# Kernel tuning notes

Hardware: AMD Instinct MI355X
Metric: run time of the kernel (lower is better)

The kernel has to match this reference:

```python
import jax, jax.numpy as jnp
import numpy as np

B, N, DX, DZ, L = 512, 32, 78, 64, 1000

def _gcn_norm(A):
    # PyG gcn_norm: add remaining self loops (fill 1), symmetric D^-1/2 (A+I) D^-1/2
    n = A.shape[-1]
    A_hat = jnp.maximum(A, jnp.eye(n, dtype=A.dtype))
    dinv = jax.lax.rsqrt(A_hat.sum(-1))
    return A_hat * dinv[..., :, None] * dinv[..., None, :]

def _bn(h, g, b, eps=1e-5):
    # BatchNorm1d, training-mode batch statistics (torch default module state)
    m = jnp.mean(h, 0)
    v = jnp.var(h, 0)
    return (h - m) * jax.lax.rsqrt(v + eps) * g + b

def _conv(h, W, b):  # h [B,C,L], W [O,I,K], valid padding + ReLU (Conv1dReLU)
    y = jax.lax.conv_general_dilated(h, W, (1,), 'VALID', dimension_numbers=('NCH', 'OIH', 'NCH'))
    return jax.nn.relu(y + b[None, :, None])

def _attn(v):  # Attention.project is only Tanh in the source
    return jax.nn.softmax(jnp.tanh(v), axis=1) * v

def _forward(x, adj, target, z, dec_W0, dec_b0, dec_g0, dec_be0, dec_W1, dec_b1, dec_g1, dec_be1,
             gW1, gb1, gW2, gb2, gW3, gb3, fcg1_W, fcg1_b, fcg2_W, fcg2_b, emb,
             c10_W, c10_b, c20_W, c20_b, c21_W, c21_b, c30_W, c30_b, c31_W, c31_b, c32_W, c32_b,
             prot_W, prot_b, fc1_W, fc1_b, fc2_W, fc2_b, out_W, out_b):
    Bn = B * N
    # frozen conditional VAE decoder -> augmented features (detached)
    zc = jnp.concatenate([z.reshape(Bn, DZ), x.reshape(Bn, DX)], axis=-1)
    h = jax.nn.relu(_bn(zc @ dec_W0 + dec_b0, dec_g0, dec_be0))
    aug = jnp.tanh(_bn(h @ dec_W1 + dec_b1, dec_g1, dec_be1))
    aug = jax.lax.stop_gradient(aug).reshape(B, N, DX)
    X = jnp.concatenate([aug, x], axis=-1)  # [B,N,156]
    # 1-hop / 2-hop / 3-hop adjacency patterns (spspmm -> binary power patterns)
    A1 = _gcn_norm(adj)
    A2p = (adj @ adj > 0).astype(adj.dtype)
    A3p = (A2p @ adj > 0).astype(adj.dtype)
    A2 = _gcn_norm(A2p)
    A3 = _gcn_norm(A3p)
    gcn = lambda A, hh, W, b: jax.nn.relu(A @ (hh @ W) + b)
    h1 = gcn(A1, X, gW1, gb1)
    h2 = gcn(A1, h1, gW2, gb2)
    h3 = gcn(A1, h2, gW3, gb3)
    h5 = gcn(A2, gcn(A2, X, gW1, gb1), gW2, gb2)
    h6 = gcn(A3, X, gW1, gb1)
    hg = jnp.max(jnp.concatenate([h3, h5, h6], axis=-1), axis=1)  # gmp -> [B,1092]
    xg = jax.nn.relu(hg @ fcg1_W + fcg1_b) @ fcg2_W + fcg2_b  # dropout = identity (eval)
    xg = _attn(xg)
    # protein branch
    e = jnp.transpose(emb[target], (0, 2, 1))  # [B,128,1000]
    f1 = jnp.max(_conv(e, c10_W, c10_b), axis=-1)
    f2 = jnp.max(_conv(_conv(e, c20_W, c20_b), c21_W, c21_b), axis=-1)
    f3 = jnp.max(_conv(_conv(_conv(e, c30_W, c30_b), c31_W, c31_b), c32_W, c32_b), axis=-1)
    xt = _attn(jnp.concatenate([f1, f2, f3], axis=-1) @ prot_W + prot_b)
    xc = jnp.concatenate([xg, xt], axis=-1)
    xc = jax.nn.relu(xc @ fc1_W + fc1_b)
    xc = jax.nn.relu(xc @ fc2_W + fc2_b)
    return xc @ out_W + out_b

def setup_inputs():
    key = jax.random.key(0)
    ks = iter(jax.random.split(key, 64))
    def w(shape, s=0.05):
        return jax.random.normal(next(ks), shape, dtype=jnp.float32) * s
    x = jax.random.normal(next(ks), (B, N, DX), dtype=jnp.float32)
    r = jax.random.uniform(next(ks), (B, N, N))
    up = jnp.triu((r < 0.08).astype(jnp.float32), 1)
    adj = up + jnp.swapaxes(up, 1, 2)  # symmetric, no self loops, avg degree ~5
    target = jax.random.randint(next(ks), (B, L), 0, 26, dtype=jnp.int32)
    z = jax.random.normal(next(ks), (B, N, DZ), dtype=jnp.float32)
    emb = w((26, 128), 1.0).at[0].set(0.0)  # padding_idx=0
    return dict(x=x, adj=adj, target=target, z=z,
        dec_W0=w((DZ + DX, 256)), dec_b0=jnp.zeros(256), dec_g0=jnp.ones(256), dec_be0=jnp.zeros(256),
        dec_W1=w((256, DX)), dec_b1=jnp.zeros(DX), dec_g1=jnp.ones(DX), dec_be1=jnp.zeros(DX),
        gW1=w((156, 156)), gb1=jnp.zeros(156), gW2=w((156, 312)), gb2=jnp.zeros(312),
        gW3=w((312, 624)), gb3=jnp.zeros(624),
        fcg1_W=w((1092, 1024)), fcg1_b=jnp.zeros(1024), fcg2_W=w((1024, 128)), fcg2_b=jnp.zeros(128),
        emb=emb,
        c10_W=w((96, 128, 3)), c10_b=jnp.zeros(96),
        c20_W=w((96, 128, 3)), c20_b=jnp.zeros(96), c21_W=w((96, 96, 3)), c21_b=jnp.zeros(96),
        c30_W=w((96, 128, 3)), c30_b=jnp.zeros(96), c31_W=w((96, 96, 3)), c31_b=jnp.zeros(96),
        c32_W=w((96, 96, 3)), c32_b=jnp.zeros(96),
        prot_W=w((288, 128)), prot_b=jnp.zeros(128),
        fc1_W=w((256, 1024)), fc1_b=jnp.zeros(1024), fc2_W=w((1024, 512)), fc2_b=jnp.zeros(512),
        out_W=w((512, 1)), out_b=jnp.zeros(1))

def reference(x, adj, target, z, dec_W0, dec_b0, dec_g0, dec_be0, dec_W1, dec_b1, dec_g1, dec_be1,
              gW1, gb1, gW2, gb2, gW3, gb3, fcg1_W, fcg1_b, fcg2_W, fcg2_b, emb,
              c10_W, c10_b, c20_W, c20_b, c21_W, c21_b, c30_W, c30_b, c31_W, c31_b, c32_W, c32_b,
              prot_W, prot_b, fc1_W, fc1_b, fc2_W, fc2_b, out_W, out_b):
    return _forward(x, adj, target, z, dec_W0, dec_b0, dec_g0, dec_be0, dec_W1, dec_b1, dec_g1, dec_be1,
                    gW1, gb1, gW2, gb2, gW3, gb3, fcg1_W, fcg1_b, fcg2_W, fcg2_b, emb,
                    c10_W, c10_b, c20_W, c20_b, c21_W, c21_b, c30_W, c30_b, c31_W, c31_b, c32_W, c32_b,
                    prot_W, prot_b, fc1_W, fc1_b, fc2_W, fc2_b, out_W, out_b)
```

## Files before the change

kernel.cpp:

```cpp
#include <hip/hip_runtime.h>

static constexpr size_t O_H0    = 0;
static constexpr size_t O_H1P   = 4194304;
static constexpr size_t O_X     = 5473216;
static constexpr size_t O_A1    = 8029120;
static constexpr size_t O_A2    = 8553408;
static constexpr size_t O_A3    = 9077696;
static constexpr size_t O_H4    = 9601984;
static constexpr size_t O_H6    = 12157888;
static constexpr size_t O_H1W2  = 14713792;
static constexpr size_t O_H2    = 19825600;
static constexpr size_t O_H2W3  = 24937408;
static constexpr size_t O_H3    = 35161024;
static constexpr size_t O_HG    = 45384640;
static constexpr size_t O_FCG1O = 45943744;
static constexpr size_t O_M     = 46468032;
static constexpr size_t O_F     = 46535424;
static constexpr size_t O_V     = 46682880;
static constexpr size_t O_XC    = 46748416;
static constexpr size_t O_FC1O  = 46879488;
static constexpr size_t O_FC2O  = 47403776;
static constexpr size_t O_PART  = 47665920;
static constexpr size_t O_MV    = 47698688;
static constexpr size_t O_BT21  = 47699712;
static constexpr size_t O_BT31  = 47727360;
static constexpr size_t O_W32T  = 47755008;
static constexpr size_t O_XW1  = O_H0;
static constexpr size_t O_SK   = O_H0;
static constexpr size_t O_H1   = O_X;
static constexpr size_t O_H4W2 = O_H1W2;
static constexpr size_t O_H5   = O_H2W3;
static constexpr size_t O_R10  = O_H1W2;
static constexpr size_t O_R20  = O_H1W2 + 1687296;
static constexpr size_t O_R30  = O_H1W2 + 3374592;
static constexpr size_t O_N21  = O_H2W3;
static constexpr size_t O_N31  = O_H2W3 + 5061888;

template<int AMODE, int ACT>
__global__ __launch_bounds__(256) void gemm_k(
    const float* __restrict__ A, const float* __restrict__ Bm,
    const float* __restrict__ bias, float* __restrict__ C,
    int M, int N, int K, const float* __restrict__ A2)
{
  __shared__ __align__(16) float sA[16 * 68];
  __shared__ __align__(16) float sB[16 * 68];
  const int tid = threadIdx.x;
  const int m0 = blockIdx.y * 64, n0 = blockIdx.x * 64;
  const int tx = tid & 15, ty = tid >> 4;
  float acc[4][4] = {};
  for (int k0 = 0; k0 < K; k0 += 16) {
#pragma unroll
    for (int s2 = 0; s2 < 4; s2++) {
      int idx = tid + s2 * 256;
      int am = idx >> 4, ak = idx & 15;
      int gm = m0 + am, gk = k0 + ak;
      float va = 0.f;
      if (gm < M && gk < K) {
        if (AMODE == 0) va = A[(size_t)gm * K + gk];
        else            va = (gk < 64) ? A[gm * 64 + gk] : A2[gm * 78 + gk - 64];
      }
      sA[ak * 68 + am] = va;
      int bk2 = idx >> 6, bn = idx & 63;
      int gk2 = k0 + bk2, gn = n0 + bn;
      float vb = 0.f;
      if (gk2 < K && gn < N) vb = Bm[(size_t)gk2 * N + gn];
      sB[bk2 * 68 + bn] = vb;
    }
    __syncthreads();
#pragma unroll
    for (int kk = 0; kk < 16; kk++) {
      const float4 a4 = *(const float4*)&sA[kk * 68 + ty * 4];
      const float4 b4 = *(const float4*)&sB[kk * 68 + tx * 4];
      const float ra[4] = {a4.x, a4.y, a4.z, a4.w};
      const float rb[4] = {b4.x, b4.y, b4.z, b4.w};
#pragma unroll
      for (int i2 = 0; i2 < 4; i2++)
#pragma unroll
        for (int j2 = 0; j2 < 4; j2++)
          acc[i2][j2] = fmaf(ra[i2], rb[j2], acc[i2][j2]);
    }
    __syncthreads();
  }
#pragma unroll
  for (int i2 = 0; i2 < 4; i2++) {
    int gm = m0 + ty * 4 + i2;
    if (gm >= M) continue;
#pragma unroll
    for (int j2 = 0; j2 < 4; j2++) {
      int gn = n0 + tx * 4 + j2;
      if (gn >= N) continue;
      float v = acc[i2][j2];
      if (bias) v += bias[gn];
      if (ACT == 1) v = fmaxf(v, 0.f);
      C[(size_t)gm * N + gn] = v;
    }
  }
}

__global__ __launch_bounds__(256) void gemm_sk(
    const float* __restrict__ A, const float* __restrict__ Bm,
    float* __restrict__ PT, int M, int N, int K, int KS)
{
  __shared__ __align__(16) float sA[16 * 68];
  __shared__ __align__(16) float sB[16 * 68];
  const int tid = threadIdx.x;
  const int m0 = blockIdx.y * 64, n0 = blockIdx.x * 64;
  const int kb = blockIdx.z * KS;
  const int ke = min(K, kb + KS);
  const int tx = tid & 15, ty = tid >> 4;
  float acc[4][4] = {};
  for (int k0 = kb; k0 < ke; k0 += 16) {
#pragma unroll
    for (int s2 = 0; s2 < 4; s2++) {
      int idx = tid + s2 * 256;
      int am = idx >> 4, ak = idx & 15;
      int gm = m0 + am, gk = k0 + ak;
      float va = 0.f;
      if (gm < M && gk < ke) va = A[(size_t)gm * K + gk];
      sA[ak * 68 + am] = va;
      int bk2 = idx >> 6, bn = idx & 63;
      int gk2 = k0 + bk2, gn = n0 + bn;
      float vb = 0.f;
      if (gk2 < ke && gn < N) vb = Bm[(size_t)gk2 * N + gn];
      sB[bk2 * 68 + bn] = vb;
    }
    __syncthreads();
#pragma unroll
    for (int kk = 0; kk < 16; kk++) {
      const float4 a4 = *(const float4*)&sA[kk * 68 + ty * 4];
      const float4 b4 = *(const float4*)&sB[kk * 68 + tx * 4];
      const float ra[4] = {a4.x, a4.y, a4.z, a4.w};
      const float rb[4] = {b4.x, b4.y, b4.z, b4.w};
#pragma unroll
      for (int i2 = 0; i2 < 4; i2++)
#pragma unroll
        for (int j2 = 0; j2 < 4; j2++)
          acc[i2][j2] = fmaf(ra[i2], rb[j2], acc[i2][j2]);
    }
    __syncthreads();
  }
  float* P = PT + (size_t)blockIdx.z * M * N;
#pragma unroll
  for (int i2 = 0; i2 < 4; i2++) {
    int gm = m0 + ty * 4 + i2;
    if (gm >= M) continue;
#pragma unroll
    for (int j2 = 0; j2 < 4; j2++) {
      int gn = n0 + tx * 4 + j2;
      if (gn >= N) continue;
      P[(size_t)gm * N + gn] = acc[i2][j2];
    }
  }
}

__global__ void skred_kernel(const float* __restrict__ PT, const float* __restrict__ bias,
                             float* __restrict__ C, int MN, int nmask, int S, int act)
{
  int i = blockIdx.x * 256 + threadIdx.x;
  if (i >= MN) return;
  float s = 0.f;
  for (int z = 0; z < S; z++) s += PT[(size_t)z * MN + i];
  if (bias) s += bias[i & nmask];
  if (act) s = fmaxf(s, 0.f);
  C[i] = s;
}

template<int AMODE, int ACT>
__global__ __launch_bounds__(256) void gemm2_k(
    const float* __restrict__ A, const float* __restrict__ Bm,
    const float* __restrict__ bias, float* __restrict__ C,
    int M, int N, int K, const float* __restrict__ A2)
{
  __shared__ __align__(16) float sA[16 * 132];
  __shared__ __align__(16) float sB[16 * 68];
  const int tid = threadIdx.x;
  const int m0 = blockIdx.y * 128, n0 = blockIdx.x * 64;
  const int tx = tid & 15, ty = tid >> 4;
  float acc[8][4] = {};
  for (int k0 = 0; k0 < K; k0 += 16) {
#pragma unroll
    for (int s2 = 0; s2 < 2; s2++) {
      int idx = tid + s2 * 256;
      int am = idx >> 2, kq = idx & 3;
      int gm = m0 + am;
#pragma unroll
      for (int j = 0; j < 4; j++) {
        int gk = k0 + kq * 4 + j;
        float va = 0.f;
        if (gm < M && gk < K) {
          if (AMODE == 0) va = A[(size_t)gm * K + gk];
          else            va = (gk < 64) ? A[gm * 64 + gk] : A2[gm * 78 + gk - 64];
        }
        sA[(kq * 4 + j) * 132 + am] = va;
      }
    }
    {
      int bk = tid >> 4, bn4 = tid & 15;
      int gk2 = k0 + bk;
#pragma unroll
      for (int j = 0; j < 4; j++) {
        int gn = n0 + bn4 * 4 + j;
        float vb = 0.f;
        if (gk2 < K && gn < N) vb = Bm[(size_t)gk2 * N + gn];
        sB[bk * 68 + bn4 * 4 + j] = vb;
      }
    }
    __syncthreads();
#pragma unroll
    for (int kk = 0; kk < 16; kk++) {
      const float4 a0 = *(const float4*)&sA[kk * 132 + ty * 8];
      const float4 a1 = *(const float4*)&sA[kk * 132 + ty * 8 + 4];
      const float4 b4 = *(const float4*)&sB[kk * 68 + tx * 4];
      const float ra[8] = {a0.x, a0.y, a0.z, a0.w, a1.x, a1.y, a1.z, a1.w};
      const float rb[4] = {b4.x, b4.y, b4.z, b4.w};
#pragma unroll
      for (int i2 = 0; i2 < 8; i2++)
#pragma unroll
        for (int j2 = 0; j2 < 4; j2++)
          acc[i2][j2] = fmaf(ra[i2], rb[j2], acc[i2][j2]);
    }
    __syncthreads();
  }
#pragma unroll
  for (int i2 = 0; i2 < 8; i2++) {
    int gm = m0 + ty * 8 + i2;
    if (gm >= M) continue;
#pragma unroll
    for (int j2 = 0; j2 < 4; j2++) {
      int gn = n0 + tx * 4 + j2;
      if (gn >= N) continue;
      float v = acc[i2][j2];
      if (bias) v += bias[gn];
      if (ACT == 1) v = fmaxf(v, 0.f);
      C[(size_t)gm * N + gn] = v;
    }
  }
}

template<int AMODE, int ACT>
__global__ __launch_bounds__(256) void gemm3_k(
    const float* __restrict__ A, const float* __restrict__ Bm,
    const float* __restrict__ bias, float* __restrict__ C,
    int M, int N, int K, const float* __restrict__ A2)
{
  __shared__ __align__(16) float sA[16][132];
  __shared__ __align__(16) float sB[16][132];
  const int tid = threadIdx.x;
  const int m0 = blockIdx.y * 128, n0 = blockIdx.x * 128;
  const int tx = tid & 15, ty = tid >> 4;
  float acc[8][8] = {};
  for (int k0 = 0; k0 < K; k0 += 16) {
    {
      int am = tid >> 1;
      int kq = (tid & 1) * 8;
      int gm = m0 + am;
#pragma unroll
      for (int j = 0; j < 8; j++) {
        int gk = k0 + kq + j;
        float va = 0.f;
        if (gm < M && gk < K) {
          if (AMODE == 0) va = A[(size_t)gm * K + gk];
          else            va = (gk < 64) ? A[gm * 64 + gk] : A2[gm * 78 + gk - 64];
        }
        sA[kq + j][am] = va;
      }
      int bk = tid >> 4;
      int bn = (tid & 15) * 8;
      int gk2 = k0 + bk;
#pragma unroll
      for (int j = 0; j < 8; j++) {
        int gn = n0 + bn + j;
        float vb = 0.f;
        if (gk2 < K && gn < N) vb = Bm[(size_t)gk2 * N + gn];
        sB[bk][bn + j] = vb;
      }
    }
    __syncthreads();
#pragma unroll
    for (int kk = 0; kk < 16; kk++) {
      const float4 a0 = *(const float4*)&sA[kk][ty * 4];
      const float4 a1 = *(const float4*)&sA[kk][64 + ty * 4];
      const float4 b0 = *(const float4*)&sB[kk][tx * 4];
      const float4 b1 = *(const float4*)&sB[kk][64 + tx * 4];
      const float ra[8] = {a0.x, a0.y, a0.z, a0.w, a1.x, a1.y, a1.z, a1.w};
      const float rb[8] = {b0.x, b0.y, b0.z, b0.w, b1.x, b1.y, b1.z, b1.w};
#pragma unroll
      for (int i = 0; i < 8; i++)
#pragma unroll
        for (int j = 0; j < 8; j++)
          acc[i][j] = fmaf(ra[i], rb[j], acc[i][j]);
    }
    __syncthreads();
  }
#pragma unroll
  for (int i = 0; i < 8; i++) {
    int gm = m0 + (i < 4 ? ty * 4 + i : 64 + ty * 4 + (i - 4));
    if (gm >= M) continue;
#pragma unroll
    for (int j = 0; j < 8; j++) {
      int gn = n0 + (j < 4 ? tx * 4 + j : 64 + tx * 4 + (j - 4));
      if (gn >= N) continue;
      float v = acc[i][j];
      if (bias) v += bias[gn];
      if (ACT == 1) v = fmaxf(v, 0.f);
      C[(size_t)gm * N + gn] = v;
    }
  }
}

__global__ __launch_bounds__(256) void bn_partial(const float* __restrict__ H,
    float* __restrict__ PS, float* __restrict__ PQ, int C)
{
  int c = blockIdx.x * 64 + (threadIdx.x & 63);
  int rg = threadIdx.x >> 6;
  __shared__ float sS[256], sQ[256];
  float s = 0.f, q = 0.f;
  if (c < C) {
    int base = blockIdx.y * 256 + rg;
    for (int t = 0; t < 64; t++) {
      float v = H[(size_t)(base + 4 * t) * C + c];
      s += v; q += v * v;
    }
  }
  sS[threadIdx.x] = s; sQ[threadIdx.x] = q;
  __syncthreads();
  if (threadIdx.x < 64 && c < C) {
    float ts = sS[threadIdx.x] + sS[threadIdx.x + 64] + sS[threadIdx.x + 128] + sS[threadIdx.x + 192];
    float tq = sQ[threadIdx.x] + sQ[threadIdx.x + 64] + sQ[threadIdx.x + 128] + sQ[threadIdx.x + 192];
    PS[blockIdx.y * C + c] = ts;
    PQ[blockIdx.y * C + c] = tq;
  }
}

__global__ void bn_final(const float* __restrict__ PS, const float* __restrict__ PQ,
                         float* __restrict__ MV, int C)
{
  int c = threadIdx.x;
  if (c >= C) return;
  float s = 0.f, q = 0.f;
  for (int y = 0; y < 64; y++) { s += PS[y * C + c]; q += PQ[y * C + c]; }
  float mean = s * (1.f / 16384.f);
  float var = q * (1.f / 16384.f) - mean * mean;
  MV[c] = mean; MV[256 + c] = var;
}

__global__ void bn_norm(const float* __restrict__ IN, float* __restrict__ OUT,
                        const float* __restrict__ MV, const float* __restrict__ g,
                        const float* __restrict__ bb, int C, int ostride, int total, int act)
{
  int idx = blockIdx.x * 256 + threadIdx.x;
  if (idx >= total) return;
  int r = idx / C, c = idx - r * C;
  float v = (IN[idx] - MV[c]) * (1.f / sqrtf(MV[256 + c] + 1e-5f)) * g[c] + bb[c];
  v = (act == 1) ? fmaxf(v, 0.f) : tanhf(v);
  OUT[(size_t)r * ostride + c] = v;
}

__global__ void xcopy_kernel(const float* __restrict__ x, float* __restrict__ X)
{
  int idx = blockIdx.x * 256 + threadIdx.x;
  if (idx >= 16384 * 78) return;
  int r = idx / 78, j = idx - r * 78;
  X[(size_t)r * 156 + 78 + j] = x[idx];
}

__global__ __launch_bounds__(1024) void adj_kernel(const float* __restrict__ adj,
    float* __restrict__ A1o, float* __restrict__ A2o, float* __restrict__ A3o)
{
  int b = blockIdx.x, t = threadIdx.x;
  int i = t >> 5, j = t & 31;
  __shared__ float sA[32][33], sP[32][33];
  __shared__ float sd1[32], sd2[32], sd3[32];
  float a = adj[b * 1024 + t];
  sA[i][j] = a;
  float ah = (i == j) ? fmaxf(a, 1.f) : a;
  float rs = ah;
#pragma unroll
  for (int m = 16; m >= 1; m >>= 1) rs += __shfl_xor(rs, m, 32);
  float di = 1.f / sqrtf(rs);
  if (j == 0) sd1[i] = di;
  __syncthreads();
  A1o[b * 1024 + t] = ah * di * sd1[j];
  float c2 = 0.f;
#pragma unroll
  for (int k = 0; k < 32; k++) c2 += sA[i][k] * sA[k][j];
  float p2 = (c2 > 0.f) ? 1.f : 0.f;
  sP[i][j] = p2;
  float ah2 = (i == j) ? 1.f : p2;
  float rs2 = ah2;
#pragma unroll
  for (int m = 16; m >= 1; m >>= 1) rs2 += __shfl_xor(rs2, m, 32);
  float di2 = 1.f / sqrtf(rs2);
  if (j == 0) sd2[i] = di2;
  __syncthreads();
  A2o[b * 1024 + t] = ah2 * di2 * sd2[j];
  float c3 = 0.f;
#pragma unroll
  for (int k = 0; k < 32; k++) c3 += sP[i][k] * sA[k][j];
  float p3 = (c3 > 0.f) ? 1.f : 0.f;
  float ah3 = (i == j) ? 1.f : p3;
  float rs3 = ah3;
#pragma unroll
  for (int m = 16; m >= 1; m >>= 1) rs3 += __shfl_xor(rs3, m, 32);
  float di3 = 1.f / sqrtf(rs3);
  if (j == 0) sd3[i] = di3;
  __syncthreads();
  A3o[b * 1024 + t] = ah3 * di3 * sd3[j];
}

__global__ __launch_bounds__(64) void agg_kernel(const float* __restrict__ A,
    const float* __restrict__ HW, const float* __restrict__ bias,
    float* __restrict__ OUT, int C)
{
  int b = blockIdx.y;
  int c = blockIdx.x * 64 + threadIdx.x;
  __shared__ float sAd[1024];
  for (int e = threadIdx.x; e < 1024; e += 64) sAd[e] = A[b * 1024 + e];
  __syncthreads();
  if (c >= C) return;
  float hw[32];
  const float* hp = HW + (size_t)b * 32 * C + c;
#pragma unroll
  for (int m = 0; m < 32; m++) hw[m] = hp[(size_t)m * C];
  float bv = bias[c];
#pragma unroll 2
  for (int n = 0; n < 32; n++) {
    float s = bv;
#pragma unroll
    for (int m = 0; m < 32; m++) s = fmaf(sAd[n * 32 + m], hw[m], s);
    OUT[(size_t)b * 32 * C + (size_t)n * C + c] = fmaxf(s, 0.f);
  }
}

__global__ void hg_kernel(const float* __restrict__ h3, const float* __restrict__ h5,
                          const float* __restrict__ h6, float* __restrict__ HG)
{
  int b = blockIdx.y;
  int c = blockIdx.x * 256 + threadIdx.x;
  if (c >= 1092) return;
  const float* p; int stride;
  if (c < 624)      { p = h3 + (size_t)b * 32 * 624 + c;          stride = 624; }
  else if (c < 936) { p = h5 + (size_t)b * 32 * 312 + (c - 624);  stride = 312; }
  else              { p = h6 + (size_t)b * 32 * 156 + (c - 936);  stride = 156; }
  float m = p[0];
#pragma unroll 4
  for (int n = 1; n < 32; n++) m = fmaxf(m, p[(size_t)n * stride]);
  HG[b * 1092 + c] = m;
}

__global__ __launch_bounds__(64) void attn_kernel(const float* __restrict__ V,
    float* __restrict__ OUT, int ostride, int ooff)
{
  int r = blockIdx.x, lane = threadIdx.x;
  float v0 = V[r * 128 + lane], v1 = V[r * 128 + 64 + lane];
  float e0 = expf(tanhf(v0)), e1 = expf(tanhf(v1));
  float s = e0 + e1;
#pragma unroll
  for (int m = 32; m >= 1; m >>= 1) s += __shfl_xor(s, m);
  float inv = 1.f / s;
  OUT[r * ostride + ooff + lane] = e0 * inv * v0;
  OUT[r * ostride + ooff + 64 + lane] = e1 * inv * v1;
}

__global__ void mtable_kernel(const float* __restrict__ emb, const float* __restrict__ W10,
    const float* __restrict__ W20, const float* __restrict__ W30, float* __restrict__ M)
{
  int idx = blockIdx.x * 256 + threadIdx.x;
  if (idx >= 3 * 3 * 26 * 96) return;
  int o = idx % 96, tok = (idx / 96) % 26, k = (idx / (96 * 26)) % 3, cv = idx / (96 * 26 * 3);
  const float* W = (cv == 0) ? W10 : ((cv == 1) ? W20 : W30);
  float s = 0.f;
#pragma unroll 4
  for (int i = 0; i < 128; i++) s = fmaf(emb[tok * 128 + i], W[(o * 128 + i) * 3 + k], s);
  M[idx] = s;
}

__global__ void rtable_kernel(const float* __restrict__ M,
    const float* __restrict__ b1, const float* __restrict__ b2, const float* __restrict__ b3,
    float* __restrict__ R1, float* __restrict__ R2, float* __restrict__ R3)
{
  int cv = blockIdx.y;
  int idx = blockIdx.x * 256 + threadIdx.x;
  if (idx >= 17576 * 96) return;
  int o = idx % 96, g = idx / 96;
  int t0 = g / 676, t1 = (g / 26) % 26, t2 = g % 26;
  const float* Mc = M + cv * 3 * 26 * 96;
  float v = ((cv == 0) ? b1 : ((cv == 1) ? b2 : b3))[o];
  v += Mc[(0 * 26 + t0) * 96 + o] + Mc[(1 * 26 + t1) * 96 + o] + Mc[(2 * 26 + t2) * 96 + o];
  float* R = (cv == 0) ? R1 : ((cv == 1) ? R2 : R3);
  R[idx] = fmaxf(v, 0.f);
}

__global__ void wtrans_kernel(const float* __restrict__ W, float* __restrict__ out, int mode)
{
  int e = blockIdx.x * 256 + threadIdx.x;
  if (e >= 96 * 96 * 3) return;
  int o, i, k;
  if (mode == 0) { i = e / 288; int r = e % 288; k = r / 96; o = r % 96; }
  else           { k = e / (96 * 96); i = (e / 96) % 96; o = e % 96; }
  out[e] = W[(o * 96 + i) * 3 + k];
}

__global__ __launch_bounds__(128) void fmax12_scan(const int* __restrict__ target,
    const float* __restrict__ R10, const float* __restrict__ N21, const float* __restrict__ b21,
    float* __restrict__ F)
{
  int b = blockIdx.x;
  const int CH = 125;
  int l0 = blockIdx.y * CH;
  int n1 = min(998 - l0, CH);
  int n2 = min(996 - l0, CH);
  int tid = threadIdx.x;
  __shared__ int sG[127];
  int ng = (n2 > 0) ? max(n1, n2 + 2) : n1;
  for (int p = tid; p < ng; p += 128) {
    int t0 = target[b * 1000 + l0 + p];
    int t1 = target[b * 1000 + l0 + p + 1];
    int t2 = target[b * 1000 + l0 + p + 2];
    sG[p] = (t0 * 26 + t1) * 26 + t2;
  }
  __syncthreads();
  int o = tid;
  if (o >= 96) return;
  float bv = b21[o];
  float m1 = 0.f, m2 = 0.f;
  for (int c = 0; c < n1; c++) {
    m1 = fmaxf(m1, R10[(size_t)sG[c] * 96 + o]);
    if (c < n2) {
      float v = bv + N21[((size_t)sG[c]     * 3 + 0) * 96 + o]
                   + N21[((size_t)sG[c + 1] * 3 + 1) * 96 + o]
                   + N21[((size_t)sG[c + 2] * 3 + 2) * 96 + o];
      m2 = fmaxf(m2, fmaxf(v, 0.f));
    }
  }
  atomicMax((unsigned int*)&F[b * 288 + o], __float_as_uint(m1));
  atomicMax((unsigned int*)&F[b * 288 + 96 + o], __float_as_uint(m2));
}

__global__ __launch_bounds__(256) void conv3_kernel(const int* __restrict__ target,
    const float* __restrict__ N31, const float* __restrict__ b31,
    const float* __restrict__ W32t, const float* __restrict__ b32, float* __restrict__ F)
{
  int b = blockIdx.y, tile = blockIdx.x;
  int l0 = tile * 64;
  int tid = threadIdx.x;
  __shared__ float sIn[96 * 67];
  __shared__ int sG[68];
  int ncols = min(66, 996 - l0);
  int nouts = min(64, 994 - l0);
  for (int p = tid; p < ncols + 2; p += 256) {
    int t0 = target[b * 1000 + l0 + p];
    int t1 = target[b * 1000 + l0 + p + 1];
    int t2 = target[b * 1000 + l0 + p + 2];
    sG[p] = (t0 * 26 + t1) * 26 + t2;
  }
  __syncthreads();
  for (int e = tid; e < 96 * ncols; e += 256) {
    int i = e % 96, c = e / 96;
    float v = b31[i]
            + N31[((size_t)sG[c]     * 3 + 0) * 96 + i]
            + N31[((size_t)sG[c + 1] * 3 + 1) * 96 + i]
            + N31[((size_t)sG[c + 2] * 3 + 2) * 96 + i];
    sIn[i * 67 + c] = fmaxf(v, 0.f);
  }
  __syncthreads();
  int wv = __builtin_amdgcn_readfirstlane(tid >> 6);
  int lane = tid & 63;
  int obase = wv * 24;
  float acc[24];
#pragma unroll
  for (int jj = 0; jj < 24; jj++) acc[jj] = b32[obase + jj];
#pragma unroll 1
  for (int k = 0; k < 3; k++) {
#pragma unroll 4
    for (int i = 0; i < 96; i++) {
      float xv = sIn[i * 67 + lane + k];
      const float* wp = W32t + ((size_t)(k * 96 + i)) * 96 + obase;
#pragma unroll
      for (int jj = 0; jj < 24; jj++) acc[jj] = fmaf(xv, wp[jj], acc[jj]);
    }
  }
  bool lok = lane < nouts;
#pragma unroll
  for (int jj = 0; jj < 24; jj++) {
    float v = lok ? fmaxf(acc[jj], 0.f) : 0.f;
#pragma unroll
    for (int m = 32; m >= 1; m >>= 1) v = fmaxf(v, __shfl_xor(v, m));
    if (lane == 0) atomicMax((unsigned int*)&F[b * 288 + 192 + obase + jj], __float_as_uint(v));
  }
}

__global__ __launch_bounds__(256) void outdot_kernel(const float* __restrict__ X,
    const float* __restrict__ W, const float* __restrict__ bptr, float* __restrict__ out)
{
  int r = blockIdx.x * 4 + (threadIdx.x >> 6);
  int lane = threadIdx.x & 63;
  float s = 0.f;
  for (int j = lane; j < 512; j += 64) s = fmaf(X[(size_t)r * 512 + j], W[j], s);
#pragma unroll
  for (int m = 32; m >= 1; m >>= 1) s += __shfl_xor(s, m);
  if (lane == 0) out[r] = s + bptr[0];
}

static inline void gemm(hipStream_t st, int AMODE, int ACT,
                        const float* A, const float* B, const float* bias, float* C,
                        int M, int N, int K, const float* A2 = nullptr)
{
  dim3 g((N + 63) / 64, (M + 63) / 64), blk(256);
  if (AMODE == 0 && ACT == 0)      gemm_k<0, 0><<<g, blk, 0, st>>>(A, B, bias, C, M, N, K, A2);
  else if (AMODE == 0 && ACT == 1) gemm_k<0, 1><<<g, blk, 0, st>>>(A, B, bias, C, M, N, K, A2);
  else                             gemm_k<1, 0><<<g, blk, 0, st>>>(A, B, bias, C, M, N, K, A2);
}

static inline void gemm2(hipStream_t st, int AMODE, int ACT,
                         const float* A, const float* B, const float* bias, float* C,
                         int M, int N, int K, const float* A2 = nullptr)
{
  dim3 g((N + 63) / 64, (M + 127) / 128), blk(256);
  if (AMODE == 0 && ACT == 0)      gemm2_k<0, 0><<<g, blk, 0, st>>>(A, B, bias, C, M, N, K, A2);
  else if (AMODE == 0 && ACT == 1) gemm2_k<0, 1><<<g, blk, 0, st>>>(A, B, bias, C, M, N, K, A2);
  else                             gemm2_k<1, 0><<<g, blk, 0, st>>>(A, B, bias, C, M, N, K, A2);
}

static inline void gemm3(hipStream_t st, int AMODE, int ACT,
                         const float* A, const float* B, const float* bias, float* C,
                         int M, int N, int K, const float* A2 = nullptr)
{
  dim3 g((N + 127) / 128, (M + 127) / 128), blk(256);
  if (AMODE == 0 && ACT == 0)      gemm3_k<0, 0><<<g, blk, 0, st>>>(A, B, bias, C, M, N, K, A2);
  else if (AMODE == 0 && ACT == 1) gemm3_k<0, 1><<<g, blk, 0, st>>>(A, B, bias, C, M, N, K, A2);
  else                             gemm3_k<1, 0><<<g, blk, 0, st>>>(A, B, bias, C, M, N, K, A2);
}

static inline void gemm_splitk(hipStream_t st, const float* A, const float* B,
                               const float* bias, float* C, int M, int N, int K,
                               int S, int act, float* PT)
{
  int KS = (K + S - 1) / S;
  dim3 g((N + 63) / 64, (M + 63) / 64, S);
  gemm_sk<<<g, 256, 0, st>>>(A, B, PT, M, N, K, KS);
  int MN = M * N;
  skred_kernel<<<(MN + 255) / 256, 256, 0, st>>>(PT, bias, C, MN, N - 1, S, act);
}

extern "C" void kernel_launch(void* const* d_in, const int* in_sizes, int n_in,
                              void* d_out, int out_size, void* d_ws, size_t ws_size,
                              hipStream_t stream)
{
  (void)in_sizes; (void)n_in; (void)out_size; (void)ws_size;
  const float* x      = (const float*)d_in[0];
  const float* adj    = (const float*)d_in[1];
  const int*   target = (const int*)  d_in[2];
  const float* z      = (const float*)d_in[3];
  const float* dec_W0 = (const float*)d_in[4];
  const float* dec_b0 = (const float*)d_in[5];
  const float* dec_g0 = (const float*)d_in[6];
  const float* dec_be0= (const float*)d_in[7];
  const float* dec_W1 = (const float*)d_in[8];
  const float* dec_b1 = (const float*)d_in[9];
  const float* dec_g1 = (const float*)d_in[10];
  const float* dec_be1= (const float*)d_in[11];
  const float* gW1    = (const float*)d_in[12];
  const float* gb1    = (const float*)d_in[13];
  const float* gW2    = (const float*)d_in[14];
  const float* gb2    = (const float*)d_in[15];
  const float* gW3    = (const float*)d_in[16];
  const float* gb3    = (const float*)d_in[17];
  const float* fcg1_W = (const float*)d_in[18];
  const float* fcg1_b = (const float*)d_in[19];
  const float* fcg2_W = (const float*)d_in[20];
  const float* fcg2_b = (const float*)d_in[21];
  const float* emb    = (const float*)d_in[22];
  const float* c10_W  = (const float*)d_in[23];
  const float* c10_b  = (const float*)d_in[24];
  const float* c20_W  = (const float*)d_in[25];
  const float* c20_b  = (const float*)d_in[26];
  const float* c21_W  = (const float*)d_in[27];
  const float* c21_b  = (const float*)d_in[28];
  const float* c30_W  = (const float*)d_in[29];
  const float* c30_b  = (const float*)d_in[30];
  const float* c31_W  = (const float*)d_in[31];
  const float* c31_b  = (const float*)d_in[32];
  const float* c32_W  = (const float*)d_in[33];
  const float* c32_b  = (const float*)d_in[34];
  const float* prot_W = (const float*)d_in[35];
  const float* prot_b = (const float*)d_in[36];
  const float* fc1_W  = (const float*)d_in[37];
  const float* fc1_b  = (const float*)d_in[38];
  const float* fc2_W  = (const float*)d_in[39];
  const float* fc2_b  = (const float*)d_in[40];
  const float* out_W  = (const float*)d_in[41];
  const float* out_b  = (const float*)d_in[42];
  float* out = (float*)d_out;
  float* ws = (float*)d_ws;

  float* H0   = ws + O_H0;   float* H1P  = ws + O_H1P;  float* X    = ws + O_X;
  float* A1   = ws + O_A1;   float* A2   = ws + O_A2;   float* A3   = ws + O_A3;
  float* XW1  = ws + O_XW1;  float* H1   = ws + O_H1;   float* H4   = ws + O_H4;
  float* H6   = ws + O_H6;   float* H1W2 = ws + O_H1W2; float* H2   = ws + O_H2;
  float* H2W3 = ws + O_H2W3; float* H3   = ws + O_H3;   float* H4W2 = ws + O_H4W2;
  float* H5   = ws + O_H5;   float* HG   = ws + O_HG;   float* FCG1O= ws + O_FCG1O;
  float* Mt   = ws + O_M;    float* F    = ws + O_F;    float* V    = ws + O_V;
  float* XC   = ws + O_XC;   float* FC1O = ws + O_FC1O; float* FC2O = ws + O_FC2O;
  float* PS   = ws + O_PART; float* PQ   = ws + O_PART + 16384;
  float* MV   = ws + O_MV;   float* SK   = ws + O_SK;
  float* R10  = ws + O_R10;  float* R20  = ws + O_R20;  float* R30  = ws + O_R30;
  float* N21  = ws + O_N21;  float* N31  = ws + O_N31;
  float* BT21 = ws + O_BT21; float* BT31 = ws + O_BT31; float* W32T = ws + O_W32T;

  gemm3(stream, 1, 0, z, dec_W0, dec_b0, H0, 16384, 256, 142, x);
  bn_partial<<<dim3(4, 64), 256, 0, stream>>>(H0, PS, PQ, 256);
  bn_final<<<1, 256, 0, stream>>>(PS, PQ, MV, 256);
  bn_norm<<<16384, 256, 0, stream>>>(H0, H0, MV, dec_g0, dec_be0, 256, 256, 16384 * 256, 1);
  gemm2(stream, 0, 0, H0, dec_W1, dec_b1, H1P, 16384, 78, 256);
  bn_partial<<<dim3(2, 64), 256, 0, stream>>>(H1P, PS, PQ, 78);
  bn_final<<<1, 256, 0, stream>>>(PS, PQ, MV, 78);
  bn_norm<<<4995, 256, 0, stream>>>(H1P, X, MV, dec_g1, dec_be1, 78, 156, 16384 * 78, 2);
  xcopy_kernel<<<4995, 256, 0, stream>>>(x, X);

  adj_kernel<<<512, 1024, 0, stream>>>(adj, A1, A2, A3);

  gemm2(stream, 0, 0, X, gW1, nullptr, XW1, 16384, 156, 156);
  agg_kernel<<<dim3(3, 512), 64, 0, stream>>>(A1, XW1, gb1, H1, 156);
  agg_kernel<<<dim3(3, 512), 64, 0, stream>>>(A2, XW1, gb1, H4, 156);
  agg_kernel<<<dim3(3, 512), 64, 0, stream>>>(A3, XW1, gb1, H6, 156);
  gemm2(stream, 0, 0, H1, gW2, nullptr, H1W2, 16384, 312, 156);
  agg_kernel<<<dim3(5, 512), 64, 0, stream>>>(A1, H1W2, gb2, H2, 312);
  gemm3(stream, 0, 0, H2, gW3, nullptr, H2W3, 16384, 624, 312);
  agg_kernel<<<dim3(10, 512), 64, 0, stream>>>(A1, H2W3, gb3, H3, 624);
  gemm2(stream, 0, 0, H4, gW2, nullptr, H4W2, 16384, 312, 156);
  agg_kernel<<<dim3(5, 512), 64, 0, stream>>>(A2, H4W2, gb2, H5, 312);
  hg_kernel<<<dim3(5, 512), 256, 0, stream>>>(H3, H5, H6, HG);

  gemm_splitk(stream, HG, fcg1_W, fcg1_b, FCG1O, 512, 1024, 1092, 4, 1, SK);
  gemm_splitk(stream, FCG1O, fcg2_W, fcg2_b, V, 512, 128, 1024, 8, 0, SK);
  attn_kernel<<<512, 64, 0, stream>>>(V, XC, 256, 0);

  hipMemsetAsync(F, 0, 512 * 288 * sizeof(float), stream);
  mtable_kernel<<<264, 256, 0, stream>>>(emb, c10_W, c20_W, c30_W, Mt);
  rtable_kernel<<<dim3(6591, 3), 256, 0, stream>>>(Mt, c10_b, c20_b, c30_b, R10, R20, R30);
  wtrans_kernel<<<108, 256, 0, stream>>>(c21_W, BT21, 0);
  wtrans_kernel<<<108, 256, 0, stream>>>(c31_W, BT31, 0);
  wtrans_kernel<<<108, 256, 0, stream>>>(c32_W, W32T, 1);
  gemm2(stream, 0, 0, R20, BT21, nullptr, N21, 17576, 288, 96);
  gemm2(stream, 0, 0, R30, BT31, nullptr, N31, 17576, 288, 96);
  fmax12_scan<<<dim3(512, 8), 128, 0, stream>>>(target, R10, N21, c21_b, F);
  conv3_kernel<<<dim3(16, 512), 256, 0, stream>>>(target, N31, c31_b, W32T, c32_b, F);
  gemm_splitk(stream, F, prot_W, prot_b, V, 512, 128, 288, 4, 0, SK);
  attn_kernel<<<512, 64, 0, stream>>>(V, XC, 256, 128);

  gemm_splitk(stream, XC, fc1_W, fc1_b, FC1O, 512, 1024, 256, 2, 1, SK);
  gemm_splitk(stream, FC1O, fc2_W, fc2_b, FC2O, 512, 512, 1024, 4, 1, SK);
  outdot_kernel<<<128, 256, 0, stream>>>(FC2O, out_W, out_b, out);
}
```

Baseline: 1.415 ms.

## Fuse conv1/conv2 max-pool scan into conv3 kernel with 384 threads

Removes the separate fmax12_scan kernel and computes the conv1 and conv2 channel maxima inside the conv3 tile kernel, reusing the same shared gather indices. Per-tile partial maxima are reduced in shared memory and then atomically merged into F. The block grows to 384 threads (6 waves at 16 outputs each instead of 4 waves at 24), which lowers register pressure per thread. Neighbouring tiles now read overlapping columns redundantly.

After: 1.412 ms. No clear change (-0.2%).

```diff
diff --git a/kernel.cpp b/kernel.cpp
--- a/kernel.cpp
+++ b/kernel.cpp
@@ -501,43 +501,9 @@
   out[e] = W[(o * 96 + i) * 3 + k];
 }
 
-__global__ __launch_bounds__(128) void fmax12_scan(const int* __restrict__ target,
-    const float* __restrict__ R10, const float* __restrict__ N21, const float* __restrict__ b21,
-    float* __restrict__ F)
-{
-  int b = blockIdx.x;
-  const int CH = 125;
-  int l0 = blockIdx.y * CH;
-  int n1 = min(998 - l0, CH);
-  int n2 = min(996 - l0, CH);
-  int tid = threadIdx.x;
-  __shared__ int sG[127];
-  int ng = (n2 > 0) ? max(n1, n2 + 2) : n1;
-  for (int p = tid; p < ng; p += 128) {
-    int t0 = target[b * 1000 + l0 + p];
-    int t1 = target[b * 1000 + l0 + p + 1];
-    int t2 = target[b * 1000 + l0 + p + 2];
-    sG[p] = (t0 * 26 + t1) * 26 + t2;
-  }
-  __syncthreads();
-  int o = tid;
-  if (o >= 96) return;
-  float bv = b21[o];
-  float m1 = 0.f, m2 = 0.f;
-  for (int c = 0; c < n1; c++) {
-    m1 = fmaxf(m1, R10[(size_t)sG[c] * 96 + o]);
-    if (c < n2) {
-      float v = bv + N21[((size_t)sG[c]     * 3 + 0) * 96 + o]
-                   + N21[((size_t)sG[c + 1] * 3 + 1) * 96 + o]
-                   + N21[((size_t)sG[c + 2] * 3 + 2) * 96 + o];
-      m2 = fmaxf(m2, fmaxf(v, 0.f));
-    }
-  }
-  atomicMax((unsigned int*)&F[b * 288 + o], __float_as_uint(m1));
-  atomicMax((unsigned int*)&F[b * 288 + 96 + o], __float_as_uint(m2));
-}
-
-__global__ __launch_bounds__(256) void conv3_kernel(const int* __restrict__ target,
+__global__ __launch_bounds__(384) void conv3_fused(const int* __restrict__ target,
+    const float* __restrict__ R10,
+    const float* __restrict__ N21, const float* __restrict__ b21,
     const float* __restrict__ N31, const float* __restrict__ b31,
     const float* __restrict__ W32t, const float* __restrict__ b32, float* __restrict__ F)
 {
@@ -546,30 +512,54 @@
   int tid = threadIdx.x;
   __shared__ float sIn[96 * 67];
   __shared__ int sG[68];
+  __shared__ float sR1[4 * 96], sR2[4 * 96];
   int ncols = min(66, 996 - l0);
+  int n1    = min(66, 998 - l0);
   int nouts = min(64, 994 - l0);
-  for (int p = tid; p < ncols + 2; p += 256) {
+  int ng    = min(68, 998 - l0);
+  for (int p = tid; p < ng; p += 384) {
     int t0 = target[b * 1000 + l0 + p];
     int t1 = target[b * 1000 + l0 + p + 1];
     int t2 = target[b * 1000 + l0 + p + 2];
     sG[p] = (t0 * 26 + t1) * 26 + t2;
   }
   __syncthreads();
-  for (int e = tid; e < 96 * ncols; e += 256) {
-    int i = e % 96, c = e / 96;
-    float v = b31[i]
-            + N31[((size_t)sG[c]     * 3 + 0) * 96 + i]
-            + N31[((size_t)sG[c + 1] * 3 + 1) * 96 + i]
-            + N31[((size_t)sG[c + 2] * 3 + 2) * 96 + i];
-    sIn[i * 67 + c] = fmaxf(v, 0.f);
+  {
+    int i = tid % 96;
+    int coff = tid / 96;
+    float v1m = 0.f, v2m = 0.f;
+    for (int c = coff; c < n1; c += 4) {
+      v1m = fmaxf(v1m, R10[(size_t)sG[c] * 96 + i]);
+      if (c < ncols) {
+        int g0 = sG[c], g1 = sG[c + 1], g2 = sG[c + 2];
+        float n3 = b31[i]
+                 + N31[((size_t)g0 * 3 + 0) * 96 + i]
+                 + N31[((size_t)g1 * 3 + 1) * 96 + i]
+                 + N31[((size_t)g2 * 3 + 2) * 96 + i];
+        sIn[i * 67 + c] = fmaxf(n3, 0.f);
+        float n2 = b21[i]
+                 + N21[((size_t)g0 * 3 + 0) * 96 + i]
+                 + N21[((size_t)g1 * 3 + 1) * 96 + i]
+                 + N21[((size_t)g2 * 3 + 2) * 96 + i];
+        v2m = fmaxf(v2m, fmaxf(n2, 0.f));
+      }
+    }
+    sR1[coff * 96 + i] = v1m;
+    sR2[coff * 96 + i] = v2m;
   }
   __syncthreads();
+  if (tid < 192) {
+    int which = tid / 96, i = tid % 96;
+    const float* r = which ? sR2 : sR1;
+    float m = fmaxf(fmaxf(r[i], r[96 + i]), fmaxf(r[192 + i], r[288 + i]));
+    atomicMax((unsigned int*)&F[b * 288 + which * 96 + i], __float_as_uint(m));
+  }
   int wv = __builtin_amdgcn_readfirstlane(tid >> 6);
   int lane = tid & 63;
-  int obase = wv * 24;
-  float acc[24];
-#pragma unroll
-  for (int jj = 0; jj < 24; jj++) acc[jj] = b32[obase + jj];
+  int obase = wv * 16;
+  float acc[16];
+#pragma unroll
+  for (int jj = 0; jj < 16; jj++) acc[jj] = b32[obase + jj];
 #pragma unroll 1
   for (int k = 0; k < 3; k++) {
 #pragma unroll 4
@@ -577,12 +567,12 @@
       float xv = sIn[i * 67 + lane + k];
       const float* wp = W32t + ((size_t)(k * 96 + i)) * 96 + obase;
 #pragma unroll
-      for (int jj = 0; jj < 24; jj++) acc[jj] = fmaf(xv, wp[jj], acc[jj]);
+      for (int jj = 0; jj < 16; jj++) acc[jj] = fmaf(xv, wp[jj], acc[jj]);
     }
   }
   bool lok = lane < nouts;
 #pragma unroll
-  for (int jj = 0; jj < 24; jj++) {
+  for (int jj = 0; jj < 16; jj++) {
     float v = lok ? fmaxf(acc[jj], 0.f) : 0.f;
 #pragma unroll
     for (int m = 32; m >= 1; m >>= 1) v = fmaxf(v, __shfl_xor(v, m));
@@ -744,8 +734,7 @@
   wtrans_kernel<<<108, 256, 0, stream>>>(c32_W, W32T, 1);
   gemm2(stream, 0, 0, R20, BT21, nullptr, N21, 17576, 288, 96);
   gemm2(stream, 0, 0, R30, BT31, nullptr, N31, 17576, 288, 96);
-  fmax12_scan<<<dim3(512, 8), 128, 0, stream>>>(target, R10, N21, c21_b, F);
-  conv3_kernel<<<dim3(16, 512), 256, 0, stream>>>(target, N31, c31_b, W32T, c32_b, F);
+  conv3_fused<<<dim3(16, 512), 384, 0, stream>>>(target, R10, N21, c21_b, N31, c31_b, W32T, c32_b, F);
   gemm_splitk(stream, F, prot_W, prot_b, V, 512, 128, 288, 4, 0, SK);
   attn_kernel<<<512, 64, 0, stream>>>(V, XC, 256, 128);
 
```
